# Kernel tuning notes

Measured on AMD Instinct MI355X. Metric: run time of the kernel, lower is better.

## Reference

```python
import jax, jax.numpy as jnp
import numpy as np

BS, T, N, DIM = 16, 2048, 2048, 128

def setup_inputs() -> dict:
    key = jax.random.key(0)
    k1, k2, k3 = jax.random.split(key, 3)
    aud_feats = jax.random.normal(k1, (BS, T, DIM), dtype=jnp.float32)
    semantic_feats = jax.random.normal(k2, (BS, N, DIM), dtype=jnp.float32)
    W = jax.random.normal(k3, (1, 3 * DIM), dtype=jnp.float32) * 0.02
    b = jnp.zeros((1,), dtype=jnp.float32)
    return {"aud_feats": aud_feats, "semantic_feats": semantic_feats, "W": W, "b": b}


def reference(aud_feats, semantic_feats, W, b):
    # S[b,i,j] = Linear(cat(h_t, h_n, h_t*h_n)) decomposed into three rank-1 pieces
    dim = aud_feats.shape[-1]
    w1 = W[0, :dim]
    w2 = W[0, dim:2 * dim]
    w3 = W[0, 2 * dim:]
    S = (jnp.einsum('btd,d->bt', aud_feats, w1)[:, :, None]
         + jnp.einsum('bnd,d->bn', semantic_feats, w2)[:, None, :]
         + jnp.einsum('btd,bnd->btn', aud_feats * w3, semantic_feats)
         + b[0])  # [bs, t, n]
    at = jax.nn.softmax(S, axis=2)                     # attend over semantic tokens
    bw = jax.nn.softmax(jnp.max(S, axis=2), axis=1)    # [bs, t]
    h_con_a2 = jnp.einsum('bt,btd->bd', bw, aud_feats)[:, None, :]   # [bs,1,d], broadcasts
    h_con_w = jnp.einsum('btn,bnd->btd', at, semantic_feats)          # [bs,t,d]
    flow_matrix = jnp.concatenate(
        [aud_feats, h_con_w, aud_feats * h_con_w, aud_feats * h_con_a2], axis=2)
    return flow_matrix
```

## Files before the change

kernel.cpp:

```cpp
#include <hip/hip_runtime.h>
#include <stdint.h>

#define BSZ 16
#define TT  2048
#define NSEM 2048
#define DIM 128
#define ORS 1024
#define PSTR 68

typedef __attribute__((ext_vector_type(8))) short short8;
typedef __attribute__((ext_vector_type(4))) float floatx4;

__device__ __forceinline__ unsigned short f2bf(float f){
  unsigned u = __float_as_uint(f);
  return (unsigned short)((u + 0x7fffu + ((u >> 16) & 1u)) >> 16);
}
__device__ __forceinline__ void ld8f(const float* p, float* v){
  floatx4 a = *(const floatx4*)p;
  floatx4 b = *(const floatx4*)(p + 4);
  v[0]=a[0]; v[1]=a[1]; v[2]=a[2]; v[3]=a[3];
  v[4]=b[0]; v[5]=b[1]; v[6]=b[2]; v[7]=b[3];
}
__device__ __forceinline__ void gload_lds16(const unsigned short* g, unsigned short* l){
  __builtin_amdgcn_global_load_lds((const __attribute__((address_space(1))) void*)g,
                                   (__attribute__((address_space(3))) void*)l, 16, 0, 0);
}


__global__ __launch_bounds__(256) void prep_kernel(const float* __restrict__ sem,
                                                   const float* __restrict__ W,
                                                   float* __restrict__ colB,
                                                   unsigned short* __restrict__ outw){
  __shared__ unsigned short tile[DIM * 72];
  const int tid = threadIdx.x;
  const int b  = blockIdx.x >> 5;
  const int n0 = (blockIdx.x & 31) * 64;

  const int r = tid >> 2, cc = tid & 3, c = cc * 32;
  const float* src = sem + ((size_t)(b * NSEM + n0 + r)) * DIM + c;
  float v[32];
  ld8f(src, v); ld8f(src + 8, v + 8); ld8f(src + 16, v + 16); ld8f(src + 24, v + 24);
  alignas(16) unsigned short bf[32];
  float cpart = 0.f;
  #pragma unroll
  for (int j = 0; j < 32; ++j){
    bf[j] = f2bf(v[j]);
    cpart += v[j] * W[DIM + c + j];
  }
  {
    const int nblk = (n0 >> 4) + (r >> 4);
    const int l15r = r & 15;
    unsigned short* base = outw + ((size_t)(b * TT + nblk * 4 + cc)) * ORS + 512;
    const uint4* s4 = (const uint4*)bf;
    #pragma unroll
    for (int q = 0; q < 4; ++q)
      *(uint4*)(base + q * 128 + l15r * 8) = s4[q];
  }
  #pragma unroll
  for (int j = 0; j < 32; ++j) tile[(c + j) * 72 + r] = bf[j];
  cpart += __shfl_xor(cpart, 1);
  cpart += __shfl_xor(cpart, 2);
  if (cc == 0) colB[b * NSEM + n0 + r] = cpart;
  __syncthreads();

  {
    const int kt = tid >> 7, dc = (tid >> 4) & 7, l15 = tid & 15;
    const int d = dc * 16 + l15;
    const int ntile = n0 >> 6;
    unsigned short* base = outw + ((size_t)(b * TT + 512 + ntile * 16 + kt * 8 + dc)) * ORS + 512;
    #pragma unroll
    for (int q = 0; q < 4; ++q){
      uint4 tv = *(const uint4*)&tile[d * 72 + kt * 32 + q * 8];
      *(uint4*)(base + q * 128 + l15 * 8) = tv;
    }
  }
}

__global__ __launch_bounds__(256, 2) void flash_kernel(const float* __restrict__ aud,
                                                    const float* __restrict__ W,
                                                    const float* __restrict__ colB,
                                                    float* __restrict__ m_ws,
                                                    float* __restrict__ outf,
                                                    const unsigned short* __restrict__ outw){
  __shared__ alignas(16) unsigned short kvt[2][16][512];
  __shared__ alignas(16) unsigned short pbuf[4][16 * PSTR];

  const int tid  = threadIdx.x;
  const int wv   = tid >> 6;
  const int lane = tid & 63;
  const int quad = lane >> 4;
  const int l15  = lane & 15;
  const int b    = blockIdx.x >> 5;
  const int t0w  = (blockIdx.x & 31) * 64 + wv * 16;

  const unsigned short* stage = outw + (size_t)b * TT * ORS + 512 + lane * 8;

  #pragma unroll
  for (int jj = 0; jj < 4; ++jj){
    const int j = wv * 4 + jj;
    gload_lds16(stage + (size_t)j * ORS, &kvt[0][j][0]);
  }

  const float* audRow = aud + ((size_t)b * TT + t0w + l15) * DIM;
  short8 qf[4];
  float rowA_part = 0.f;
  #pragma unroll
  for (int kc = 0; kc < 4; ++kc){
    int d0 = kc * 32 + quad * 8;
    float av[8], w3v[8], w1v[8];
    ld8f(audRow + d0, av);
    ld8f(W + 2 * DIM + d0, w3v);
    ld8f(W + d0, w1v);
    alignas(16) unsigned short tmp[8];
    #pragma unroll
    for (int j = 0; j < 8; ++j){
      tmp[j] = f2bf(av[j] * w3v[j]);
      rowA_part += av[j] * w1v[j];
    }
    qf[kc] = *(const short8*)tmp;
  }
  rowA_part += __shfl_xor(rowA_part, 16);
  rowA_part += __shfl_xor(rowA_part, 32);

  float m_run = -1e30f, l_run = 0.f;
  float m_true = -1e30f;
  floatx4 o[8];
  #pragma unroll
  for (int dc = 0; dc < 8; ++dc){
    #pragma unroll
    for (int r = 0; r < 4; ++r) o[dc][r] = 0.f;
  }

  const float* colBb = colB + b * NSEM;
  unsigned short* pb = &pbuf[wv][0];

  __syncthreads();

  for (int it = 0; it < 32; ++it){
    const int n0 = it * 64;

    const int cV = 512 + it * 16;
    short8 vf[16];
    #pragma unroll
    for (int i = 0; i < 16; ++i) vf[i] = *(const short8*)(stage + (size_t)(cV + i) * ORS);

    if (it + 1 < 32){
      #pragma unroll
      for (int jj = 0; jj < 4; ++jj){
        const int j = wv * 4 + jj;
        gload_lds16(stage + (size_t)((it + 1) * 16 + j) * ORS, &kvt[(it + 1) & 1][j][0]);
      }
    }
    __builtin_amdgcn_sched_barrier(0);

    const unsigned short* kvb = &kvt[it & 1][0][0] + lane * 8;

    floatx4 cbv[4];
    #pragma unroll
    for (int s = 0; s < 4; ++s) cbv[s] = *(const floatx4*)(colBb + n0 + s*16 + quad*4);

    floatx4 sacc[4];
    #pragma unroll
    for (int s = 0; s < 4; ++s){ sacc[s][0]=0.f; sacc[s][1]=0.f; sacc[s][2]=0.f; sacc[s][3]=0.f; }
    #pragma unroll
    for (int s = 0; s < 4; ++s){
      #pragma unroll
      for (int kc = 0; kc < 4; ++kc){
        short8 kf = *(const short8*)(kvb + (s*4 + kc) * 512);
        sacc[s] = __builtin_amdgcn_mfma_f32_16x16x32_bf16(kf, qf[kc], sacc[s], 0, 0, 0);
      }
    }

    float v[4][4];
    #pragma unroll
    for (int s = 0; s < 4; ++s){
      #pragma unroll
      for (int r = 0; r < 4; ++r) v[s][r] = sacc[s][r] + cbv[s][r];
    }
    float mq[4];
    #pragma unroll
    for (int s = 0; s < 4; ++s)
      mq[s] = fmaxf(fmaxf(v[s][0], v[s][1]), fmaxf(v[s][2], v[s][3]));
    float mx = fmaxf(fmaxf(mq[0], mq[1]), fmaxf(mq[2], mq[3]));
    mx = fmaxf(mx, __shfl_xor(mx, 16));
    mx = fmaxf(mx, __shfl_xor(mx, 32));
    m_true = fmaxf(m_true, mx);

    const bool defer = (__all(mx - m_run <= 8.0f) != 0);
    float al = 1.0f;
    if (!defer){
      float mnew = fmaxf(m_run, mx);
      al = __expf(m_run - mnew);
      m_run = mnew;
    }
    float e[4][4];
    #pragma unroll
    for (int s = 0; s < 4; ++s){
      #pragma unroll
      for (int r = 0; r < 4; ++r) e[s][r] = __expf(v[s][r] - m_run);
    }
    float sq[4];
    #pragma unroll
    for (int s = 0; s < 4; ++s)
      sq[s] = (e[s][0] + e[s][1]) + (e[s][2] + e[s][3]);
    float ps = (sq[0] + sq[1]) + (sq[2] + sq[3]);
    ps += __shfl_xor(ps, 16);
    ps += __shfl_xor(ps, 32);
    l_run = l_run * al + ps;

    #pragma unroll
    for (int s = 0; s < 4; ++s){
      unsigned u0 = (unsigned)f2bf(e[s][0]) | ((unsigned)f2bf(e[s][1]) << 16);
      unsigned u1 = (unsigned)f2bf(e[s][2]) | ((unsigned)f2bf(e[s][3]) << 16);
      unsigned short* pr = pb + l15 * PSTR + s * 16 + quad * 4;
      *(unsigned*)(pr)     = u0;
      *(unsigned*)(pr + 2) = u1;
    }

    if (!defer){
      float aB[4];
      #pragma unroll
      for (int r = 0; r < 4; ++r) aB[r] = __shfl(al, quad*4 + r);
      #pragma unroll
      for (int dc = 0; dc < 8; ++dc){
        #pragma unroll
        for (int r = 0; r < 4; ++r) o[dc][r] *= aB[r];
      }
    }

    asm volatile("s_waitcnt lgkmcnt(0)" ::: "memory");
    short8 pf0 = *(const short8*)(pb + l15 * PSTR + quad * 8);
    short8 pf1 = *(const short8*)(pb + l15 * PSTR + 32 + quad * 8);

    #pragma unroll
    for (int kt = 0; kt < 2; ++kt){
      short8 pf = kt ? pf1 : pf0;
      #pragma unroll
      for (int dc = 0; dc < 8; ++dc)
        o[dc] = __builtin_amdgcn_mfma_f32_16x16x32_bf16(pf, vf[kt*8 + dc], o[dc], 0, 0, 0);
    }

    __syncthreads();
  }

  float rl = 1.0f / l_run;
  float rB[4];
  #pragma unroll
  for (int r = 0; r < 4; ++r) rB[r] = __shfl(rl, quad*4 + r);
  float* outB = outf + ((size_t)b * TT + t0w) * 512 + 128;
  #pragma unroll
  for (int dc = 0; dc < 8; ++dc){
    #pragma unroll
    for (int r = 0; r < 4; ++r)
      outB[(size_t)(quad*4 + r) * 512 + dc*16 + l15] = o[dc][r] * rB[r];
  }
  if (quad == 0)
    m_ws[(size_t)b * TT + t0w + l15] = m_true + rowA_part;
}

__global__ __launch_bounds__(256) void bw1_kernel(const float* __restrict__ m_ws,
                                                  float* __restrict__ pmax){
  __shared__ float sA[4];
  const int b = blockIdx.x >> 3, ch = blockIdx.x & 7, tid = threadIdx.x;
  float v = m_ws[(size_t)b * TT + ch * 256 + tid];
  #pragma unroll
  for (int off = 1; off < 64; off <<= 1) v = fmaxf(v, __shfl_xor(v, off));
  if ((tid & 63) == 0) sA[tid >> 6] = v;
  __syncthreads();
  if (tid == 0)
    pmax[blockIdx.x] = fmaxf(fmaxf(sA[0], sA[1]), fmaxf(sA[2], sA[3]));
}

__global__ __launch_bounds__(256) void bw2_kernel(const float* __restrict__ aud,
                                                  const float* __restrict__ m_ws,
                                                  const float* __restrict__ pmax,
                                                  float* __restrict__ gpart,
                                                  float* __restrict__ part){
  __shared__ float wbuf[256];
  __shared__ float red[16 * 128];
  __shared__ float gs4[4];
  const int b = blockIdx.x >> 3, ch = blockIdx.x & 7, tid = threadIdx.x;

  float gmax = pmax[b * 8];
  #pragma unroll
  for (int i = 1; i < 8; ++i) gmax = fmaxf(gmax, pmax[b * 8 + i]);

  float w = __expf(m_ws[(size_t)b * TT + ch * 256 + tid] - gmax);
  wbuf[tid] = w;
  float sm = w;
  #pragma unroll
  for (int off = 1; off < 64; off <<= 1) sm += __shfl_xor(sm, off);
  if ((tid & 63) == 0) gs4[tid >> 6] = sm;
  __syncthreads();
  if (tid == 0) gpart[blockIdx.x] = (gs4[0] + gs4[1]) + (gs4[2] + gs4[3]);

  const int dg = tid & 15, q = tid >> 4;
  float acc[8] = {0,0,0,0,0,0,0,0};
  const float* ab = aud + ((size_t)b * TT + ch * 256 + q * 16) * DIM + dg * 8;
  for (int i = 0; i < 16; ++i){
    float av[8];
    ld8f(ab + (size_t)i * DIM, av);
    float wt = wbuf[q * 16 + i];
    #pragma unroll
    for (int j = 0; j < 8; ++j) acc[j] += wt * av[j];
  }
  #pragma unroll
  for (int j = 0; j < 8; ++j) red[q * 128 + dg * 8 + j] = acc[j];
  __syncthreads();
  if (tid < 128){
    float s = 0.f;
    #pragma unroll
    for (int q2 = 0; q2 < 16; ++q2) s += red[q2 * 128 + tid];
    part[(size_t)blockIdx.x * 128 + tid] = s;
  }
}

__global__ __launch_bounds__(256) void epi_kernel(const float* __restrict__ aud,
                                                  const float* __restrict__ gpart,
                                                  const float* __restrict__ part,
                                                  float* __restrict__ out){
  __shared__ float a2s[DIM];
  int id = blockIdx.x * 256 + threadIdx.x;
  int c = id & 15;
  int t = (id >> 4) & (TT - 1);
  int b = id >> 15;
  size_t row = (size_t)b * TT + t;

  if (threadIdx.x < 128){
    const int d = threadIdx.x;
    float s = 0.f, g = 0.f;
    #pragma unroll
    for (int ch = 0; ch < 8; ++ch){
      s += part[(size_t)(b * 8 + ch) * 128 + d];
      g += gpart[b * 8 + ch];
    }
    a2s[d] = s / g;
  }
  __syncthreads();

  float av[8], gv[8], hv[8];
  ld8f(aud + row * DIM + c * 8, av);
  ld8f(out + row * 512 + 128 + c * 8, hv);
  #pragma unroll
  for (int j = 0; j < 8; ++j) gv[j] = a2s[c * 8 + j];

  floatx4 o0a, o0b, o2a, o2b, o3a, o3b;
  #pragma unroll
  for (int j = 0; j < 4; ++j){
    o0a[j] = av[j];           o0b[j] = av[4+j];
    o2a[j] = av[j]*hv[j];     o2b[j] = av[4+j]*hv[4+j];
    o3a[j] = av[j]*gv[j];     o3b[j] = av[4+j]*gv[4+j];
  }
  float* ob = out + row * 512 + c * 8;
  *(floatx4*)(ob)       = o0a;  *(floatx4*)(ob + 4)   = o0b;
  *(floatx4*)(ob + 256) = o2a;  *(floatx4*)(ob + 260) = o2b;
  *(floatx4*)(ob + 384) = o3a;  *(floatx4*)(ob + 388) = o3b;
}

extern "C" void kernel_launch(void* const* d_in, const int* in_sizes, int n_in,
                              void* d_out, int out_size, void* d_ws, size_t ws_size,
                              hipStream_t stream){
  const float* aud = (const float*)d_in[0];
  const float* sem = (const float*)d_in[1];
  const float* W   = (const float*)d_in[2];
  float* out = (float*)d_out;
  unsigned short* outw = (unsigned short*)d_out;

  float* ws    = (float*)d_ws;
  float* m_ws  = ws;
  float* colB  = m_ws + (size_t)BSZ * TT;
  float* a2_ws = colB + (size_t)BSZ * NSEM;
  float* pmax  = a2_ws + BSZ * DIM;
  float* gpart = pmax + 128;
  float* part  = gpart + 128;

  prep_kernel <<<512, 256, 0, stream>>>(sem, W, colB, outw);
  flash_kernel<<<512, 256, 0, stream>>>(aud, W, colB, m_ws, out, outw);
  bw1_kernel  <<<128, 256, 0, stream>>>(m_ws, pmax);
  bw2_kernel  <<<128, 256, 0, stream>>>(aud, m_ws, pmax, gpart, part);
  epi_kernel  <<<(BSZ * TT * 16) / 256, 256, 0, stream>>>(aud, gpart, part, out);
}
```

Baseline: 197.3 us.

## Use exp2 softmax, packed bf16 convert, inline V loads, fold bw1 into flash via atomicMax

The log2e factor is folded into the query weights and column bias so the softmax can use the native exp2 instead of __expf. The e values are packed with v_cvt_pk_bf16_f32, and V fragments are fetched with inline-asm global loads plus an explicit partial vmcnt wait. The separate bw1 max-reduction kernel is removed; each flash wave now does an atomicMax on an order-preserving uint key, which needs an added memset launch. The prefetch now wraps on the last iteration, issuing one redundant load, and the hand-written waitcnt relies on the compiler's load ordering.

```diff
diff --git a/kernel.cpp b/kernel.cpp
--- a/kernel.cpp
+++ b/kernel.cpp
@@ -7,6 +7,8 @@
 #define DIM 128
 #define ORS 1024
 #define PSTR 68
+#define LOG2E 1.4426950408889634f
+#define LN2   0.6931471805599453f
 
 typedef __attribute__((ext_vector_type(8))) short short8;
 typedef __attribute__((ext_vector_type(4))) float floatx4;
@@ -14,6 +16,18 @@
 __device__ __forceinline__ unsigned short f2bf(float f){
   unsigned u = __float_as_uint(f);
   return (unsigned short)((u + 0x7fffu + ((u >> 16) & 1u)) >> 16);
+}
+__device__ __forceinline__ unsigned pkbf(float a, float b){
+  unsigned r;
+  asm("v_cvt_pk_bf16_f32 %0, %1, %2" : "=v"(r) : "v"(a), "v"(b));
+  return r;
+}
+__device__ __forceinline__ float e2(float x){
+#if __has_builtin(__builtin_amdgcn_exp2f)
+  return __builtin_amdgcn_exp2f(x);
+#else
+  return exp2f(x);
+#endif
 }
 __device__ __forceinline__ void ld8f(const float* p, float* v){
   floatx4 a = *(const floatx4*)p;
@@ -24,6 +38,20 @@
 __device__ __forceinline__ void gload_lds16(const unsigned short* g, unsigned short* l){
   __builtin_amdgcn_global_load_lds((const __attribute__((address_space(1))) void*)g,
                                    (__attribute__((address_space(3))) void*)l, 16, 0, 0);
+}
+__device__ __forceinline__ short8 gld16(const unsigned short* p){
+  short8 r;
+  asm volatile("global_load_dwordx4 %0, %1, off"
+               : "=v"(r) : "v"(p) : "memory");
+  return r;
+}
+__device__ __forceinline__ unsigned fkey(float f){
+  unsigned u = __float_as_uint(f);
+  return u ^ ((unsigned)((int)u >> 31) | 0x80000000u);
+}
+__device__ __forceinline__ float fdec(unsigned k){
+  unsigned u = (k & 0x80000000u) ? (k ^ 0x80000000u) : ~k;
+  return __uint_as_float(u);
 }
 
 
@@ -60,7 +88,7 @@
   for (int j = 0; j < 32; ++j) tile[(c + j) * 72 + r] = bf[j];
   cpart += __shfl_xor(cpart, 1);
   cpart += __shfl_xor(cpart, 2);
-  if (cc == 0) colB[b * NSEM + n0 + r] = cpart;
+  if (cc == 0) colB[b * NSEM + n0 + r] = cpart * LOG2E;
   __syncthreads();
 
   {
@@ -81,7 +109,8 @@
                                                     const float* __restrict__ colB,
                                                     float* __restrict__ m_ws,
                                                     float* __restrict__ outf,
-                                                    const unsigned short* __restrict__ outw){
+                                                    const unsigned short* __restrict__ outw,
+                                                    unsigned* __restrict__ pmax_u){
   __shared__ alignas(16) unsigned short kvt[2][16][512];
   __shared__ alignas(16) unsigned short pbuf[4][16 * PSTR];
 
@@ -114,7 +143,7 @@
     alignas(16) unsigned short tmp[8];
     #pragma unroll
     for (int j = 0; j < 8; ++j){
-      tmp[j] = f2bf(av[j] * w3v[j]);
+      tmp[j] = f2bf(av[j] * (w3v[j] * LOG2E));
       rowA_part += av[j] * w1v[j];
     }
     qf[kc] = *(const short8*)tmp;
@@ -139,25 +168,26 @@
   for (int it = 0; it < 32; ++it){
     const int n0 = it * 64;
 
+    floatx4 cbv[4];
+    #pragma unroll
+    for (int s = 0; s < 4; ++s) cbv[s] = *(const floatx4*)(colBb + n0 + s*16 + quad*4);
+
     const int cV = 512 + it * 16;
     short8 vf[16];
     #pragma unroll
-    for (int i = 0; i < 16; ++i) vf[i] = *(const short8*)(stage + (size_t)(cV + i) * ORS);
-
-    if (it + 1 < 32){
+    for (int i = 0; i < 16; ++i) vf[i] = gld16(stage + (size_t)(cV + i) * ORS);
+
+    {
+      const int itn = (it + 1) & 31;
       #pragma unroll
       for (int jj = 0; jj < 4; ++jj){
         const int j = wv * 4 + jj;
-        gload_lds16(stage + (size_t)((it + 1) * 16 + j) * ORS, &kvt[(it + 1) & 1][j][0]);
+        gload_lds16(stage + (size_t)(itn * 16 + j) * ORS, &kvt[(it + 1) & 1][j][0]);
       }
     }
     __builtin_amdgcn_sched_barrier(0);
 
     const unsigned short* kvb = &kvt[it & 1][0][0] + lane * 8;
-
-    floatx4 cbv[4];
-    #pragma unroll
-    for (int s = 0; s < 4; ++s) cbv[s] = *(const floatx4*)(colBb + n0 + s*16 + quad*4);
 
     floatx4 sacc[4];
     #pragma unroll
@@ -190,14 +220,14 @@
     float al = 1.0f;
     if (!defer){
       float mnew = fmaxf(m_run, mx);
-      al = __expf(m_run - mnew);
+      al = e2(m_run - mnew);
       m_run = mnew;
     }
     float e[4][4];
     #pragma unroll
     for (int s = 0; s < 4; ++s){
       #pragma unroll
-      for (int r = 0; r < 4; ++r) e[s][r] = __expf(v[s][r] - m_run);
+      for (int r = 0; r < 4; ++r) e[s][r] = e2(v[s][r] - m_run);
     }
     float sq[4];
     #pragma unroll
@@ -210,8 +240,8 @@
 
     #pragma unroll
     for (int s = 0; s < 4; ++s){
-      unsigned u0 = (unsigned)f2bf(e[s][0]) | ((unsigned)f2bf(e[s][1]) << 16);
-      unsigned u1 = (unsigned)f2bf(e[s][2]) | ((unsigned)f2bf(e[s][3]) << 16);
+      unsigned u0 = pkbf(e[s][0], e[s][1]);
+      unsigned u1 = pkbf(e[s][2], e[s][3]);
       unsigned short* pr = pb + l15 * PSTR + s * 16 + quad * 4;
       *(unsigned*)(pr)     = u0;
       *(unsigned*)(pr + 2) = u1;
@@ -232,6 +262,9 @@
     short8 pf0 = *(const short8*)(pb + l15 * PSTR + quad * 8);
     short8 pf1 = *(const short8*)(pb + l15 * PSTR + 32 + quad * 8);
 
+    asm volatile("s_waitcnt vmcnt(4)" ::: "memory");
+    __builtin_amdgcn_sched_barrier(0);
+
     #pragma unroll
     for (int kt = 0; kt < 2; ++kt){
       short8 pf = kt ? pf1 : pf0;
@@ -254,26 +287,19 @@
     for (int r = 0; r < 4; ++r)
       outB[(size_t)(quad*4 + r) * 512 + dc*16 + l15] = o[dc][r] * rB[r];
   }
+  float mval = m_true * LN2 + rowA_part;
   if (quad == 0)
-    m_ws[(size_t)b * TT + t0w + l15] = m_true + rowA_part;
-}
-
-__global__ __launch_bounds__(256) void bw1_kernel(const float* __restrict__ m_ws,
-                                                  float* __restrict__ pmax){
-  __shared__ float sA[4];
-  const int b = blockIdx.x >> 3, ch = blockIdx.x & 7, tid = threadIdx.x;
-  float v = m_ws[(size_t)b * TT + ch * 256 + tid];
-  #pragma unroll
-  for (int off = 1; off < 64; off <<= 1) v = fmaxf(v, __shfl_xor(v, off));
-  if ((tid & 63) == 0) sA[tid >> 6] = v;
-  __syncthreads();
-  if (tid == 0)
-    pmax[blockIdx.x] = fmaxf(fmaxf(sA[0], sA[1]), fmaxf(sA[2], sA[3]));
+    m_ws[(size_t)b * TT + t0w + l15] = mval;
+  mval = fmaxf(mval, __shfl_xor(mval, 1));
+  mval = fmaxf(mval, __shfl_xor(mval, 2));
+  mval = fmaxf(mval, __shfl_xor(mval, 4));
+  mval = fmaxf(mval, __shfl_xor(mval, 8));
+  if (lane == 0) atomicMax(pmax_u + b, fkey(mval));
 }
 
 __global__ __launch_bounds__(256) void bw2_kernel(const float* __restrict__ aud,
                                                   const float* __restrict__ m_ws,
-                                                  const float* __restrict__ pmax,
+                                                  const unsigned* __restrict__ pmax_u,
                                                   float* __restrict__ gpart,
                                                   float* __restrict__ part){
   __shared__ float wbuf[256];
@@ -281,9 +307,7 @@
   __shared__ float gs4[4];
   const int b = blockIdx.x >> 3, ch = blockIdx.x & 7, tid = threadIdx.x;
 
-  float gmax = pmax[b * 8];
-  #pragma unroll
-  for (int i = 1; i < 8; ++i) gmax = fmaxf(gmax, pmax[b * 8 + i]);
+  float gmax = fdec(pmax_u[b]);
 
   float w = __expf(m_ws[(size_t)b * TT + ch * 256 + tid] - gmax);
   wbuf[tid] = w;
@@ -366,17 +390,17 @@
   float* out = (float*)d_out;
   unsigned short* outw = (unsigned short*)d_out;
 
-  float* ws    = (float*)d_ws;
-  float* m_ws  = ws;
-  float* colB  = m_ws + (size_t)BSZ * TT;
-  float* a2_ws = colB + (size_t)BSZ * NSEM;
-  float* pmax  = a2_ws + BSZ * DIM;
-  float* gpart = pmax + 128;
-  float* part  = gpart + 128;
-
+  float* ws      = (float*)d_ws;
+  float* m_ws    = ws;
+  float* colB    = m_ws + (size_t)BSZ * TT;
+  float* a2_ws   = colB + (size_t)BSZ * NSEM;
+  unsigned* pmax_u = (unsigned*)(a2_ws + BSZ * DIM);
+  float* gpart   = (float*)pmax_u + 128;
+  float* part    = gpart + 128;
+
+  hipMemsetAsync(pmax_u, 0, BSZ * sizeof(unsigned), stream);
   prep_kernel <<<512, 256, 0, stream>>>(sem, W, colB, outw);
-  flash_kernel<<<512, 256, 0, stream>>>(aud, W, colB, m_ws, out, outw);
-  bw1_kernel  <<<128, 256, 0, stream>>>(m_ws, pmax);
-  bw2_kernel  <<<128, 256, 0, stream>>>(aud, m_ws, pmax, gpart, part);
+  flash_kernel<<<512, 256, 0, stream>>>(aud, W, colB, m_ws, out, outw, pmax_u);
+  bw2_kernel  <<<128, 256, 0, stream>>>(aud, m_ws, pmax_u, gpart, part);
   epi_kernel  <<<(BSZ * TT * 16) / 256, 256, 0, stream>>>(aud, gpart, part, out);
 }
```

After: 200.2 us. No clear change (+1.5%).
